# Optimization experiments

Hardware: AMD Instinct MI355X
Metric: run time of the kernel (lower is better)

## Reference

```python
import jax, jax.numpy as jnp
import numpy as np

SCORE_THR = 0.01
IOU_THR = 0.1          # NOTE: original layer hardcodes 0.1 in tf.image.non_max_suppression
MAX_DET = 100
NEG = jnp.float32(-1e30)


def _iou_one_vs_all(box, boxes):
    # box: [4] (y1,x1,y2,x2), boxes: [N,4]
    y1 = jnp.maximum(box[0], boxes[:, 0])
    x1 = jnp.maximum(box[1], boxes[:, 1])
    y2 = jnp.minimum(box[2], boxes[:, 2])
    x2 = jnp.minimum(box[3], boxes[:, 3])
    inter = jnp.maximum(y2 - y1, 0.0) * jnp.maximum(x2 - x1, 0.0)
    a = (box[2] - box[0]) * (box[3] - box[1])
    b = (boxes[:, 2] - boxes[:, 0]) * (boxes[:, 3] - boxes[:, 1])
    return inter / (a + b - inter + 1e-8)


def _nms_keep(boxes, scores):
    # Greedy NMS as a keep-mask over N anchors. Matches tf.image.non_max_suppression
    # restricted to anchors with score > SCORE_THR, up to MAX_DET selections.
    s = jnp.where(scores > SCORE_THR, scores, NEG)
    keep0 = jnp.zeros(s.shape, dtype=bool)

    def step(carry, _):
        s, keep = carry
        i = jnp.argmax(s)
        ok = s[i] > NEG * 0.5
        keep = keep.at[i].set(ok)
        iou = _iou_one_vs_all(boxes[i], boxes)
        s = jnp.where((iou > IOU_THR) & ok, NEG, s)
        s = s.at[i].set(NEG)
        return (s, keep), None

    (_, keep), _ = jax.lax.scan(step, (s, keep0), None, length=MAX_DET)
    return keep


def _filter_image(boxes_i, cls_i):
    # boxes_i: [N,4], cls_i: [N,C]
    C = cls_i.shape[1]
    # class-specific NMS: keep mask per class -> [C, N]
    keep = jax.vmap(lambda s: _nms_keep(boxes_i, s))(cls_i.T)
    keep_flat = keep.T.reshape(-1)          # [N*C], (anchor, class) flat order
    flat = cls_i.reshape(-1)                # [N*C]
    masked = jnp.where(keep_flat, flat, NEG)
    vals, idx = jax.lax.top_k(masked, MAX_DET)
    valid = vals > NEG * 0.5
    anchor = idx // C
    label = idx % C
    scores_out = jnp.where(valid, jnp.take(flat, idx), -1.0)
    boxes_out = jnp.where(valid[:, None], boxes_i[anchor], -1.0)
    labels_out = jnp.where(valid, label, -1).astype(jnp.int32)
    return boxes_out, scores_out, labels_out


def setup_inputs() -> dict:
    key = jax.random.key(0)
    k1, k2, k3 = jax.random.split(key, 3)
    B, N, C = 4, 49104, 90
    yx1 = jax.random.uniform(k1, (B, N, 2), dtype=jnp.float32) * 512.0
    hw = jax.random.uniform(k2, (B, N, 2), dtype=jnp.float32) * 128.0 + 1.0
    boxes = jnp.concatenate([yx1, yx1 + hw], axis=-1)          # [B,N,4] y1x1y2x2
    classification = jax.random.uniform(k3, (B, N, C), dtype=jnp.float32)
    return {"boxes": boxes, "classification": classification}


def reference(boxes, classification):
    return jax.vmap(_filter_image)(boxes, classification)
```

## Files before the change

kernel.cpp:

```cpp
#include <hip/hip_runtime.h>
#include <stdint.h>

typedef unsigned long long u64;

#define B_ 4
#define N_ 49104
#define C_ 90
#define NCLS (B_ * C_)
#define MAXK 100
#define THR 0.01f
#define NB2 2048
#define WIN 512
#define ACH 128
#define NCH ((N_ + ACH - 1) / ACH)
#define CAPC 32
#define NBIN_M 1280
#define BINBASE 0x3F6E0000u
#define BINSH_M 10

__device__ __forceinline__ float area_of(float y1, float x1, float y2, float x2) {
#pragma clang fp contract(off)
  return (y2 - y1) * (x2 - x1);
}

#define IOU_MID (26843547.0 / 268435456.0)

__device__ __forceinline__ bool iou_gt(float ay1, float ax1, float ay2, float ax2, float aa,
                                       float by1, float bx1, float by2, float bx2, float ba) {
#pragma clang fp contract(off)
  float y1 = fmaxf(ay1, by1);
  float x1 = fmaxf(ax1, bx1);
  float y2 = fminf(ay2, by2);
  float x2 = fminf(ax2, bx2);
  float inter = fmaxf(y2 - y1, 0.0f) * fmaxf(x2 - x1, 0.0f);
  float denom = aa + ba - inter + 1e-8f;
  return (double)inter >= IOU_MID * (double)denom;
}

__device__ __forceinline__ u64 umax64(u64 a, u64 b) { return a > b ? a : b; }

__device__ __forceinline__ u64 shfl_xor_u64(u64 v, int m) {
  int lo = __shfl_xor((int)(unsigned)v, m);
  int hi = __shfl_xor((int)(unsigned)(v >> 32), m);
  return ((u64)(unsigned)hi << 32) | (u64)(unsigned)lo;
}

__device__ __forceinline__ int key2bin_m(u64 k) {
  int d = (int)((unsigned)(k >> 32) - BINBASE);
  int bin = d >> BINSH_M;
  if (d < 0) bin = 0;
  if (bin > NBIN_M - 1) bin = NBIN_M - 1;
  return bin;
}

__global__ __launch_bounds__(256) void select_kernel(const float* __restrict__ cls,
                                                     u64* __restrict__ keybuf,
                                                     unsigned* __restrict__ cnt,
                                                     int capsel, float t0) {
  __shared__ u64 ll[C_ * CAPC];
  __shared__ unsigned lcnt[C_];
  __shared__ unsigned base_s[C_];
  int blk = blockIdx.x;
  int b = blk / NCH, ch = blk - b * NCH;
  int a0 = ch * ACH;
  int aEnd = a0 + ACH; if (aEnd > N_) aEnd = N_;
  int e0 = a0 * C_;
  int nelem = (aEnd - a0) * C_;
  int tid = threadIdx.x;

  for (int i = tid; i < C_; i += 256) lcnt[i] = 0u;
  __syncthreads();

  const float4* src4 = (const float4*)(cls + (size_t)b * N_ * C_ + e0);
  int n4 = nelem >> 2;
  for (int i4 = tid; i4 < n4; i4 += 256) {
    float4 v = src4[i4];
#pragma unroll
    for (int j = 0; j < 4; ++j) {
      float s = (&v.x)[j];
      if (s > t0) {
        int e = e0 + i4 * 4 + j;
        unsigned n = (unsigned)e / (unsigned)C_;
        unsigned c = (unsigned)e - n * (unsigned)C_;
        u64 key = ((u64)__float_as_uint(s) << 32) | (u64)(0xFFFFFFFFu - n);
        unsigned pos = atomicAdd(&lcnt[c], 1u);
        if (pos < CAPC) {
          ll[c * CAPC + pos] = key;
        } else {
          unsigned g = (unsigned)(b * C_) + c;
          unsigned gp = atomicAdd(&cnt[g * 16], 1u);
          if (gp < (unsigned)capsel) keybuf[(size_t)g * capsel + gp] = key;
        }
      }
    }
  }
  __syncthreads();

  if (tid < C_) {
    unsigned cc = lcnt[tid]; if (cc > CAPC) cc = CAPC;
    base_s[tid] = atomicAdd(&cnt[(b * C_ + tid) * 16], cc);
  }
  __syncthreads();

  for (int i = tid; i < C_ * CAPC; i += 256) {
    int c = i >> 5, j = i & 31;
    unsigned cc = lcnt[c]; if (cc > CAPC) cc = CAPC;
    if ((unsigned)j < cc) {
      unsigned pos = base_s[c] + (unsigned)j;
      if (pos < (unsigned)capsel)
        keybuf[(size_t)(b * C_ + c) * capsel + pos] = ll[i];
    }
  }
}

__global__ __launch_bounds__(512) void nms_kernel(const float* __restrict__ boxes,
                                                  const float* __restrict__ cls,
                                                  const u64* __restrict__ keybuf,
                                                  const unsigned* __restrict__ cnt,
                                                  int capsel, float t0,
                                                  u64* __restrict__ keepkeys,
                                                  int* __restrict__ nk_arr) {
  int gcls = blockIdx.x;
  int b = gcls / C_, c = gcls - b * C_;
  __shared__ u64 karr[4096];
  __shared__ unsigned hist[NB2];
  __shared__ unsigned sfx[NB2];
  __shared__ float4 kb[MAXK];
  __shared__ float ka[MAXK];
  __shared__ unsigned wsum[8];
  __shared__ int sh_cnt[8];
  int tid = threadIdx.x;
  int lane = tid & 63;
  int wid = tid >> 6;

  for (int i = tid; i < MAXK; i += 512) keepkeys[(size_t)gcls * MAXK + i] = 0ull;
  for (int i = tid; i < NB2; i += 512) hist[i] = 0u;
  __syncthreads();

  unsigned Mraw = cnt[gcls * 16];
  bool overflow = (Mraw > (unsigned)capsel);
  int M = overflow ? 0 : (int)Mraw;

  const u64* src = keybuf + (size_t)gcls * capsel;

  const int PK = 4096 / 512;
  u64 kreg[PK];
#pragma unroll
  for (int q = 0; q < PK; ++q) {
    kreg[q] = 0ull;
    int i = q * 512 + tid;
    if (i < M) {
      kreg[q] = src[i];
      atomicAdd(&hist[(unsigned)(kreg[q] >> 44) & (NB2 - 1)], 1u);
    }
  }
  __syncthreads();

  {
    const int W = NB2 / 512;
    unsigned loc[W];
    unsigned psum = 0;
#pragma unroll
    for (int q = 0; q < W; ++q) {
      psum += hist[NB2 - 1 - (tid * W + q)];
      loc[q] = psum;
    }
    unsigned incl = psum;
#pragma unroll
    for (int s = 1; s < 64; s <<= 1) {
      unsigned v = (unsigned)__shfl_up((int)incl, s);
      if (lane >= s) incl += v;
    }
    if (lane == 63) wsum[wid] = incl;
    __syncthreads();
    unsigned bs = incl - psum;
    for (int w2 = 0; w2 < wid; ++w2) bs += wsum[w2];
#pragma unroll
    for (int q = 0; q < W; ++q)
      sfx[NB2 - 1 - (tid * W + q)] = bs + loc[q];
  }
  __syncthreads();

#pragma unroll
  for (int q = 0; q < PK; ++q) {
    int i = q * 512 + tid;
    if (i < M) {
      u64 k = kreg[q];
      unsigned bin = (unsigned)(k >> 44) & (NB2 - 1);
      unsigned old = atomicSub(&hist[bin], 1u);
      karr[sfx[bin] - old] = k;
    }
  }
  __syncthreads();

  {
    u64 mk2[PK]; int mt[PK];
#pragma unroll
    for (int q = 0; q < PK; ++q) {
      mk2[q] = 0ull; mt[q] = -1;
      int i = q * 512 + tid;
      if (i < M) {
        u64 k = karr[i];
        int bin = (int)((unsigned)(k >> 44) & (NB2 - 1));
        int hi2 = (int)sfx[bin];
        int lo2 = (bin == NB2 - 1) ? 0 : (int)sfx[bin + 1];
        int r = lo2;
        for (int j = lo2; j < hi2; ++j) r += (karr[j] > k);
        mk2[q] = k; mt[q] = r;
      }
    }
    __syncthreads();
#pragma unroll
    for (int q = 0; q < PK; ++q)
      if (mt[q] >= 0) karr[mt[q]] = mk2[q];
  }
  __syncthreads();

  const float4* bx4 = (const float4*)(boxes + (size_t)b * N_ * 4);

  int seen = 0;
  int nwin = (M + WIN - 1) / WIN;
  for (int w = 0; w < nwin && seen < MAXK; ++w) {
    int base = w * WIN;
    int ci = base + tid;
    bool have = ci < M;
    float4 cb = make_float4(0.f, 0.f, 0.f, 0.f);
    float ca = 0.f;
    if (have) {
      u64 k = karr[ci];
      cb = bx4[0xFFFFFFFFu - (unsigned)(k & 0xFFFFFFFFull)];
      ca = area_of(cb.x, cb.y, cb.z, cb.w);
    }
    bool dead = !have;
    for (int j = 0; j < seen; ++j) {
      float4 sb = kb[j]; float sa = ka[j];
      dead |= iou_gt(sb.x, sb.y, sb.z, sb.w, sa,
                     cb.x, cb.y, cb.z, cb.w, ca);
    }
    u64 alive = __ballot(!dead);

    int nslice = (((M - base) < WIN ? (M - base) : WIN) + 63) >> 6;
    for (int s = 0; s < nslice; ++s) {
      if (wid == s) {
        int nkl = seen;
        int slo = base + (s << 6);
        while (alive != 0ull && nkl < MAXK) {
          int bit = __ffsll((long long)alive) - 1;
          float sy1 = __shfl(cb.x, bit);
          float sx1 = __shfl(cb.y, bit);
          float sy2 = __shfl(cb.z, bit);
          float sx2 = __shfl(cb.w, bit);
          float sa  = __shfl(ca,   bit);
          if (lane == 0) {
            u64 key = karr[slo + bit];
            unsigned anchor = 0xFFFFFFFFu - (unsigned)(key & 0xFFFFFFFFull);
            unsigned flat = anchor * C_ + (unsigned)c;
            keepkeys[(size_t)gcls * MAXK + nkl] =
                (key & 0xFFFFFFFF00000000ull) | (u64)(0xFFFFFFFFu - flat);
            kb[nkl] = make_float4(sy1, sx1, sy2, sx2);
            ka[nkl] = sa;
          }
          ++nkl;
          alive &= ~__ballot(iou_gt(sy1, sx1, sy2, sx2, sa,
                                    cb.x, cb.y, cb.z, cb.w, ca));
        }
        if (lane == 0) sh_cnt[s] = nkl;
        seen = nkl;
      }
      __syncthreads();
      int nkNew = (wid == s) ? seen : sh_cnt[s];
      if (nkNew >= MAXK) { seen = nkNew; break; }
      if (wid > s && nkNew > seen) {
        bool d2 = false;
        for (int j = seen; j < nkNew; ++j) {
          float4 sb = kb[j]; float sa = ka[j];
          d2 |= iou_gt(sb.x, sb.y, sb.z, sb.w, sa,
                       cb.x, cb.y, cb.z, cb.w, ca);
        }
        alive &= __ballot(!d2);
      }
      seen = nkNew;
    }
  }

  int nkF = seen;
  if (nkF < MAXK) {
    float teff = overflow ? 2.0f : t0;
    const float* sbase = cls + (size_t)b * N_ * C_ + c;
    const float* bx = boxes + (size_t)b * N_ * 4;
    u64* kkp = keepkeys + (size_t)gcls * MAXK;
    u64* red = karr;
    int nk2 = nkF;
    while (nk2 < MAXK) {
      u64 best = 0ull;
      for (int n = tid; n < N_; n += 512) {
        float s = sbase[(size_t)n * C_];
        if (s > THR && s <= teff) {
          float y1 = bx[(size_t)n * 4 + 0], x1 = bx[(size_t)n * 4 + 1];
          float y2 = bx[(size_t)n * 4 + 2], x2 = bx[(size_t)n * 4 + 3];
          float ar = area_of(y1, x1, y2, x2);
          bool ov = false;
          for (int j = 0; j < nk2; ++j) {
            float4 kbj = kb[j];
            if (iou_gt(kbj.x, kbj.y, kbj.z, kbj.w, ka[j], y1, x1, y2, x2, ar)) { ov = true; break; }
          }
          if (!ov) {
            u64 key = ((u64)__float_as_uint(s) << 32) | (u64)(0xFFFFFFFFu - (unsigned)n);
            best = umax64(best, key);
          }
        }
      }
      red[tid] = best;
      __syncthreads();
      for (int sft = 256; sft > 0; sft >>= 1) {
        if (tid < sft) red[tid] = umax64(red[tid], red[tid + sft]);
        __syncthreads();
      }
      u64 sel = red[0];
      __syncthreads();
      if (sel == 0ull) {
        if (tid == 0) {
          unsigned target2 = 0xFFFFFFFFu - (unsigned)c;
          for (int j = 0; j < nk2; ++j)
            if ((unsigned)(kkp[j] & 0xFFFFFFFFull) == target2) kkp[j] = 0ull;
        }
        break;
      }
      unsigned anchor = 0xFFFFFFFFu - (unsigned)(sel & 0xFFFFFFFFull);
      if (tid == 0) {
        float y1 = bx[(size_t)anchor * 4 + 0], x1 = bx[(size_t)anchor * 4 + 1];
        float y2 = bx[(size_t)anchor * 4 + 2], x2 = bx[(size_t)anchor * 4 + 3];
        kb[nk2] = make_float4(y1, x1, y2, x2);
        ka[nk2] = area_of(y1, x1, y2, x2);
        unsigned flat = anchor * C_ + (unsigned)c;
        kkp[nk2] = (sel & 0xFFFFFFFF00000000ull) | (u64)(0xFFFFFFFFu - flat);
      }
      ++nk2;
      __syncthreads();
    }
    nkF = nk2;
  }
  if (tid == 0) nk_arr[gcls] = nkF;
}

__global__ __launch_bounds__(256) void merge_kernel(const float* __restrict__ boxes,
                                                    const u64* __restrict__ keepkeys,
                                                    const int* __restrict__ nk_arr,
                                                    float* __restrict__ out) {
  int b = blockIdx.x;
  int tid = threadIdx.x;
  int lane = tid & 63;
  int wid = tid >> 6;
  __shared__ unsigned hist[NBIN_M];
  __shared__ unsigned sfx[NBIN_M];
  __shared__ unsigned wsum[4];
  __shared__ u64 mk[512];
  __shared__ u64 selk[MAXK];
  __shared__ int sh_thr;
  __shared__ unsigned sh_cc;
  const u64* kk = keepkeys + (size_t)b * C_ * MAXK;
  const int TOT = C_ * MAXK;

  for (int i = tid; i < NBIN_M; i += 256) hist[i] = 0u;
  if (tid == 0) { sh_thr = -1; sh_cc = 0u; }
  __syncthreads();
  for (int i = tid; i < TOT; i += 256) {
    u64 k = kk[i];
    if (k != 0ull) atomicAdd(&hist[key2bin_m(k)], 1u);
  }
  __syncthreads();

  const int W = 5;
  int j0 = tid * W;
  unsigned psum = 0;
#pragma unroll
  for (int q = 0; q < W; ++q) {
    int bin = NBIN_M - 1 - (j0 + q);
    if (bin >= 0) psum += hist[bin];
  }
  unsigned incl = psum;
#pragma unroll
  for (int s = 1; s < 64; s <<= 1) {
    unsigned v = (unsigned)__shfl_up((int)incl, s);
    if (lane >= s) incl += v;
  }
  if (lane == 63) wsum[wid] = incl;
  __syncthreads();
  unsigned base = 0;
  for (int w2 = 0; w2 < wid; ++w2) base += wsum[w2];
  unsigned running = base + incl - psum;
  int mythr = -1;
#pragma unroll
  for (int q = 0; q < W; ++q) {
    int bin = NBIN_M - 1 - (j0 + q);
    if (bin >= 0) {
      running += hist[bin];
      sfx[bin] = running;
      if (mythr < 0 && running >= (unsigned)MAXK) mythr = bin;
    }
  }
  if (mythr >= 0) atomicMax(&sh_thr, mythr);
  __syncthreads();

  int thr = sh_thr; if (thr < 0) thr = 0;
  unsigned S = sfx[thr];

  if (S <= 512u) {
    for (int i = tid; i < TOT; i += 256) {
      u64 k = kk[i];
      if (k != 0ull && key2bin_m(k) >= thr) {
        unsigned pos = atomicAdd(&sh_cc, 1u);
        mk[pos] = k;
      }
    }
    __syncthreads();
    for (int i = (int)S + tid; i < 512; i += 256) mk[i] = 0ull;
    __syncthreads();
    for (int k2 = 2; k2 <= 512; k2 <<= 1) {
      for (int j = k2 >> 1; j > 0; j >>= 1) {
        int i1 = 2 * tid - (tid & (j - 1));
        int i2 = i1 | j;
        u64 a = mk[i1], bb2 = mk[i2];
        bool desc = ((i1 & k2) == 0);
        bool sw = desc ? (a < bb2) : (a > bb2);
        if (sw) { mk[i1] = bb2; mk[i2] = a; }
        __syncthreads();
      }
    }
    for (int r = tid; r < MAXK; r += 256) selk[r] = mk[r];
    __syncthreads();
  } else {
    if (wid == 0) {
      int c0 = lane, c1 = lane + 64;
      int len0 = (c0 < C_) ? nk_arr[b * C_ + c0] : 0;
      int len1 = (c1 < C_) ? nk_arr[b * C_ + c1] : 0;
      int h0 = 0, h1 = 0;
      auto fetchc = [&](int cc, int& h, int len) -> u64 {
        while (h < len) {
          u64 k = kk[(size_t)cc * MAXK + h];
          if (k != 0ull) return k;
          ++h;
        }
        return 0ull;
      };
      u64 cand0 = (c0 < C_) ? fetchc(c0, h0, len0) : 0ull;
      u64 cand1 = (c1 < C_) ? fetchc(c1, h1, len1) : 0ull;
      for (int r = 0; r < MAXK; ++r) {
        u64 my = umax64(cand0, cand1);
        u64 g = my;
#pragma unroll
        for (int m = 1; m < 64; m <<= 1) g = umax64(g, shfl_xor_u64(g, m));
        if (lane == 0) selk[r] = g;
        if (g != 0ull && my == g) {
          if (cand0 == g) { ++h0; cand0 = fetchc(c0, h0, len0); }
          else            { ++h1; cand1 = fetchc(c1, h1, len1); }
        }
      }
    }
    __syncthreads();
  }

  for (int r = tid; r < MAXK; r += 256) {
    u64 s = selk[r];
    float oy1, ox1, oy2, ox2, sc, lb;
    if (s != 0ull) {
      unsigned flat = 0xFFFFFFFFu - (unsigned)(s & 0xFFFFFFFFull);
      unsigned anchor = flat / C_;
      unsigned label = flat - anchor * C_;
      sc = __uint_as_float((unsigned)(s >> 32));
      const float4 bp = ((const float4*)(boxes + (size_t)b * N_ * 4))[anchor];
      oy1 = bp.x; ox1 = bp.y; oy2 = bp.z; ox2 = bp.w;
      lb = (float)label;
    } else {
      oy1 = ox1 = oy2 = ox2 = -1.0f; sc = -1.0f; lb = -1.0f;
    }
    float* bo = out + ((size_t)b * MAXK + r) * 4;
    bo[0] = oy1; bo[1] = ox1; bo[2] = oy2; bo[3] = ox2;
    out[(size_t)B_ * MAXK * 4 + b * MAXK + r] = sc;
    out[(size_t)B_ * MAXK * 4 + B_ * MAXK + b * MAXK + r] = lb;
  }
}

extern "C" void kernel_launch(void* const* d_in, const int* in_sizes, int n_in,
                              void* d_out, int out_size, void* d_ws, size_t ws_size,
                              hipStream_t stream) {
  const float* boxes = (const float*)d_in[0];
  const float* cls = (const float*)d_in[1];
  char* ws = (char*)d_ws;

  int capsel; float t0;
  auto need_for = [](int cap) -> size_t {
    return 23040 + (size_t)NCLS * cap * 8 + 288000 + 1440;
  };
  if (ws_size >= need_for(4096))      { capsel = 4096; t0 = 0.93f;  }
  else if (ws_size >= need_for(2048)) { capsel = 2048; t0 = 0.962f; }
  else                                { capsel = 1024; t0 = 0.985f; }

  unsigned* cnt = (unsigned*)ws;
  u64* keybuf = (u64*)(ws + 23040);
  size_t off = 23040 + (size_t)NCLS * capsel * 8;
  u64* keepkeys = (u64*)(ws + off);      off += 288000;
  int* nk_arr = (int*)(ws + off);

  hipMemsetAsync(cnt, 0, 23040, stream);
  select_kernel<<<B_ * NCH, 256, 0, stream>>>(cls, keybuf, cnt, capsel, t0);
  nms_kernel<<<NCLS, 512, 0, stream>>>(boxes, cls, keybuf, cnt, capsel, t0,
                                       keepkeys, nk_arr);
  merge_kernel<<<B_, 256, 0, stream>>>(boxes, keepkeys, nk_arr, (float*)d_out);
}
```

Measured before the change: 189.0 us.

## Fuse merge into NMS via last-block pattern, shrink capacity, pair greedy steps

```diff
diff --git a/kernel.cpp b/kernel.cpp
--- a/kernel.cpp
+++ b/kernel.cpp
@@ -10,13 +10,16 @@
 #define MAXK 100
 #define THR 0.01f
 #define NB2 2048
-#define WIN 512
+#define WIN 256
+#define KCAP 1024
 #define ACH 128
 #define NCH ((N_ + ACH - 1) / ACH)
 #define CAPC 32
 #define NBIN_M 1280
 #define BINBASE 0x3F6E0000u
 #define BINSH_M 10
+#define T0 0.985f
+#define CAPSEL 1024
 
 __device__ __forceinline__ float area_of(float y1, float x1, float y2, float x2) {
 #pragma clang fp contract(off)
@@ -42,6 +45,12 @@
 __device__ __forceinline__ u64 shfl_xor_u64(u64 v, int m) {
   int lo = __shfl_xor((int)(unsigned)v, m);
   int hi = __shfl_xor((int)(unsigned)(v >> 32), m);
+  return ((u64)(unsigned)hi << 32) | (u64)(unsigned)lo;
+}
+
+__device__ __forceinline__ u64 shfl_u64(u64 v, int src) {
+  int lo = __shfl((int)(unsigned)v, src);
+  int hi = __shfl((int)(unsigned)(v >> 32), src);
   return ((u64)(unsigned)hi << 32) | (u64)(unsigned)lo;
 }
 
@@ -113,42 +122,46 @@
   }
 }
 
-__global__ __launch_bounds__(512) void nms_kernel(const float* __restrict__ boxes,
+__global__ __launch_bounds__(256) void nms_kernel(const float* __restrict__ boxes,
                                                   const float* __restrict__ cls,
                                                   const u64* __restrict__ keybuf,
                                                   const unsigned* __restrict__ cnt,
+                                                  unsigned* __restrict__ done,
                                                   int capsel, float t0,
                                                   u64* __restrict__ keepkeys,
-                                                  int* __restrict__ nk_arr) {
+                                                  int* __restrict__ nk_arr,
+                                                  float* __restrict__ out) {
   int gcls = blockIdx.x;
   int b = gcls / C_, c = gcls - b * C_;
-  __shared__ u64 karr[4096];
+  __shared__ u64 karr[KCAP];
   __shared__ unsigned hist[NB2];
   __shared__ unsigned sfx[NB2];
   __shared__ float4 kb[MAXK];
   __shared__ float ka[MAXK];
-  __shared__ unsigned wsum[8];
-  __shared__ int sh_cnt[8];
+  __shared__ unsigned wsum[4];
+  __shared__ int sh_cnt[4];
+  __shared__ int sh_last, sh_thr;
+  __shared__ unsigned sh_cc;
   int tid = threadIdx.x;
   int lane = tid & 63;
   int wid = tid >> 6;
 
-  for (int i = tid; i < MAXK; i += 512) keepkeys[(size_t)gcls * MAXK + i] = 0ull;
-  for (int i = tid; i < NB2; i += 512) hist[i] = 0u;
+  for (int i = tid; i < MAXK; i += 256) keepkeys[(size_t)gcls * MAXK + i] = 0ull;
+  for (int i = tid; i < NB2; i += 256) hist[i] = 0u;
   __syncthreads();
 
   unsigned Mraw = cnt[gcls * 16];
-  bool overflow = (Mraw > (unsigned)capsel);
+  bool overflow = (Mraw > (unsigned)KCAP);
   int M = overflow ? 0 : (int)Mraw;
 
   const u64* src = keybuf + (size_t)gcls * capsel;
 
-  const int PK = 4096 / 512;
+  const int PK = KCAP / 256;
   u64 kreg[PK];
 #pragma unroll
   for (int q = 0; q < PK; ++q) {
     kreg[q] = 0ull;
-    int i = q * 512 + tid;
+    int i = q * 256 + tid;
     if (i < M) {
       kreg[q] = src[i];
       atomicAdd(&hist[(unsigned)(kreg[q] >> 44) & (NB2 - 1)], 1u);
@@ -157,7 +170,7 @@
   __syncthreads();
 
   {
-    const int W = NB2 / 512;
+    const int W = NB2 / 256;
     unsigned loc[W];
     unsigned psum = 0;
 #pragma unroll
@@ -183,7 +196,7 @@
 
 #pragma unroll
   for (int q = 0; q < PK; ++q) {
-    int i = q * 512 + tid;
+    int i = q * 256 + tid;
     if (i < M) {
       u64 k = kreg[q];
       unsigned bin = (unsigned)(k >> 44) & (NB2 - 1);
@@ -198,7 +211,7 @@
 #pragma unroll
     for (int q = 0; q < PK; ++q) {
       mk2[q] = 0ull; mt[q] = -1;
-      int i = q * 512 + tid;
+      int i = q * 256 + tid;
       if (i < M) {
         u64 k = karr[i];
         int bin = (int)((unsigned)(k >> 44) & (NB2 - 1));
@@ -224,11 +237,12 @@
     int base = w * WIN;
     int ci = base + tid;
     bool have = ci < M;
+    u64 myk = 0ull;
     float4 cb = make_float4(0.f, 0.f, 0.f, 0.f);
     float ca = 0.f;
     if (have) {
-      u64 k = karr[ci];
-      cb = bx4[0xFFFFFFFFu - (unsigned)(k & 0xFFFFFFFFull)];
+      myk = karr[ci];
+      cb = bx4[0xFFFFFFFFu - (unsigned)(myk & 0xFFFFFFFFull)];
       ca = area_of(cb.x, cb.y, cb.z, cb.w);
     }
     bool dead = !have;
@@ -243,32 +257,53 @@
     for (int s = 0; s < nslice; ++s) {
       if (wid == s) {
         int nkl = seen;
-        int slo = base + (s << 6);
         while (alive != 0ull && nkl < MAXK) {
           int bit = __ffsll((long long)alive) - 1;
-          float sy1 = __shfl(cb.x, bit);
-          float sx1 = __shfl(cb.y, bit);
-          float sy2 = __shfl(cb.z, bit);
-          float sx2 = __shfl(cb.w, bit);
-          float sa  = __shfl(ca,   bit);
+          u64 rest = alive & (alive - 1ull);
+          int nbit = __ffsll((long long)rest) - 1;
+          int pidx = nbit >= 0 ? nbit : bit;
+          float b1y1 = __shfl(cb.x, bit), b1x1 = __shfl(cb.y, bit);
+          float b1y2 = __shfl(cb.z, bit), b1x2 = __shfl(cb.w, bit);
+          float a1 = __shfl(ca, bit);
+          float b2y1 = __shfl(cb.x, pidx), b2x1 = __shfl(cb.y, pidx);
+          float b2y2 = __shfl(cb.z, pidx), b2x2 = __shfl(cb.w, pidx);
+          float a2 = __shfl(ca, pidx);
+          u64 k1 = shfl_u64(myk, bit);
+          u64 k2 = shfl_u64(myk, pidx);
+          bool kill1 = iou_gt(b1y1, b1x1, b1y2, b1x2, a1,
+                              cb.x, cb.y, cb.z, cb.w, ca);
+          bool kill2 = iou_gt(b2y1, b2x1, b2y2, b2x2, a2,
+                              cb.x, cb.y, cb.z, cb.w, ca);
+          u64 m1 = __ballot(kill1);
           if (lane == 0) {
-            u64 key = karr[slo + bit];
-            unsigned anchor = 0xFFFFFFFFu - (unsigned)(key & 0xFFFFFFFFull);
+            unsigned anchor = 0xFFFFFFFFu - (unsigned)(k1 & 0xFFFFFFFFull);
             unsigned flat = anchor * C_ + (unsigned)c;
             keepkeys[(size_t)gcls * MAXK + nkl] =
-                (key & 0xFFFFFFFF00000000ull) | (u64)(0xFFFFFFFFu - flat);
-            kb[nkl] = make_float4(sy1, sx1, sy2, sx2);
-            ka[nkl] = sa;
+                (k1 & 0xFFFFFFFF00000000ull) | (u64)(0xFFFFFFFFu - flat);
+            kb[nkl] = make_float4(b1y1, b1x1, b1y2, b1x2);
+            ka[nkl] = a1;
           }
           ++nkl;
-          alive &= ~__ballot(iou_gt(sy1, sx1, sy2, sx2, sa,
-                                    cb.x, cb.y, cb.z, cb.w, ca));
+          alive = rest & ~m1;
+          if (alive == 0ull || nkl >= MAXK) break;
+          if ((__ffsll((long long)alive) - 1) == nbit) {
+            u64 m2 = __ballot(kill2);
+            if (lane == 0) {
+              unsigned anchor = 0xFFFFFFFFu - (unsigned)(k2 & 0xFFFFFFFFull);
+              unsigned flat = anchor * C_ + (unsigned)c;
+              keepkeys[(size_t)gcls * MAXK + nkl] =
+                  (k2 & 0xFFFFFFFF00000000ull) | (u64)(0xFFFFFFFFu - flat);
+              kb[nkl] = make_float4(b2y1, b2x1, b2y2, b2x2);
+              ka[nkl] = a2;
+            }
+            ++nkl;
+            alive &= ~m2;
+          }
         }
         if (lane == 0) sh_cnt[s] = nkl;
-        seen = nkl;
-      }
-      __syncthreads();
-      int nkNew = (wid == s) ? seen : sh_cnt[s];
+      }
+      __syncthreads();
+      int nkNew = sh_cnt[s];
       if (nkNew >= MAXK) { seen = nkNew; break; }
       if (wid > s && nkNew > seen) {
         bool d2 = false;
@@ -293,7 +328,7 @@
     int nk2 = nkF;
     while (nk2 < MAXK) {
       u64 best = 0ull;
-      for (int n = tid; n < N_; n += 512) {
+      for (int n = tid; n < N_; n += 256) {
         float s = sbase[(size_t)n * C_];
         if (s > THR && s <= teff) {
           float y1 = bx[(size_t)n * 4 + 0], x1 = bx[(size_t)n * 4 + 1];
@@ -312,7 +347,7 @@
       }
       red[tid] = best;
       __syncthreads();
-      for (int sft = 256; sft > 0; sft >>= 1) {
+      for (int sft = 128; sft > 0; sft >>= 1) {
         if (tid < sft) red[tid] = umax64(red[tid], red[tid + sft]);
         __syncthreads();
       }
@@ -341,143 +376,142 @@
     nkF = nk2;
   }
   if (tid == 0) nk_arr[gcls] = nkF;
-}
-
-__global__ __launch_bounds__(256) void merge_kernel(const float* __restrict__ boxes,
-                                                    const u64* __restrict__ keepkeys,
-                                                    const int* __restrict__ nk_arr,
-                                                    float* __restrict__ out) {
-  int b = blockIdx.x;
-  int tid = threadIdx.x;
-  int lane = tid & 63;
-  int wid = tid >> 6;
-  __shared__ unsigned hist[NBIN_M];
-  __shared__ unsigned sfx[NBIN_M];
-  __shared__ unsigned wsum[4];
-  __shared__ u64 mk[512];
-  __shared__ u64 selk[MAXK];
-  __shared__ int sh_thr;
-  __shared__ unsigned sh_cc;
-  const u64* kk = keepkeys + (size_t)b * C_ * MAXK;
-  const int TOT = C_ * MAXK;
-
-  for (int i = tid; i < NBIN_M; i += 256) hist[i] = 0u;
-  if (tid == 0) { sh_thr = -1; sh_cc = 0u; }
-  __syncthreads();
-  for (int i = tid; i < TOT; i += 256) {
-    u64 k = kk[i];
-    if (k != 0ull) atomicAdd(&hist[key2bin_m(k)], 1u);
-  }
-  __syncthreads();
-
-  const int W = 5;
-  int j0 = tid * W;
-  unsigned psum = 0;
-#pragma unroll
-  for (int q = 0; q < W; ++q) {
-    int bin = NBIN_M - 1 - (j0 + q);
-    if (bin >= 0) psum += hist[bin];
-  }
-  unsigned incl = psum;
-#pragma unroll
-  for (int s = 1; s < 64; s <<= 1) {
-    unsigned v = (unsigned)__shfl_up((int)incl, s);
-    if (lane >= s) incl += v;
-  }
-  if (lane == 63) wsum[wid] = incl;
-  __syncthreads();
-  unsigned base = 0;
-  for (int w2 = 0; w2 < wid; ++w2) base += wsum[w2];
-  unsigned running = base + incl - psum;
-  int mythr = -1;
-#pragma unroll
-  for (int q = 0; q < W; ++q) {
-    int bin = NBIN_M - 1 - (j0 + q);
-    if (bin >= 0) {
-      running += hist[bin];
-      sfx[bin] = running;
-      if (mythr < 0 && running >= (unsigned)MAXK) mythr = bin;
-    }
-  }
-  if (mythr >= 0) atomicMax(&sh_thr, mythr);
-  __syncthreads();
-
-  int thr = sh_thr; if (thr < 0) thr = 0;
-  unsigned S = sfx[thr];
-
-  if (S <= 512u) {
+
+  __syncthreads();
+  if (tid == 0) {
+    __threadfence();
+    sh_last = (atomicAdd(&done[b], 1u) == (unsigned)(C_ - 1)) ? 1 : 0;
+  }
+  __syncthreads();
+  if (!sh_last) return;
+  __threadfence();
+
+  {
+    const u64* kk = keepkeys + (size_t)b * C_ * MAXK;
+    const int TOT = C_ * MAXK;
+    unsigned* histm = hist;
+    unsigned* sfxm = sfx;
+    u64* mk = karr;
+    u64* selk = karr + 512;
+
+    for (int i = tid; i < NBIN_M; i += 256) histm[i] = 0u;
+    if (tid == 0) { sh_thr = -1; sh_cc = 0u; }
+    __syncthreads();
     for (int i = tid; i < TOT; i += 256) {
       u64 k = kk[i];
-      if (k != 0ull && key2bin_m(k) >= thr) {
-        unsigned pos = atomicAdd(&sh_cc, 1u);
-        mk[pos] = k;
-      }
+      if (k != 0ull) atomicAdd(&histm[key2bin_m(k)], 1u);
     }
     __syncthreads();
-    for (int i = (int)S + tid; i < 512; i += 256) mk[i] = 0ull;
+
+    const int W = 5;
+    int j0 = tid * W;
+    unsigned psum = 0;
+#pragma unroll
+    for (int q = 0; q < W; ++q) {
+      int bin = NBIN_M - 1 - (j0 + q);
+      if (bin >= 0) psum += histm[bin];
+    }
+    unsigned incl = psum;
+#pragma unroll
+    for (int s = 1; s < 64; s <<= 1) {
+      unsigned v = (unsigned)__shfl_up((int)incl, s);
+      if (lane >= s) incl += v;
+    }
+    if (lane == 63) wsum[wid] = incl;
     __syncthreads();
-    for (int k2 = 2; k2 <= 512; k2 <<= 1) {
-      for (int j = k2 >> 1; j > 0; j >>= 1) {
-        int i1 = 2 * tid - (tid & (j - 1));
-        int i2 = i1 | j;
-        u64 a = mk[i1], bb2 = mk[i2];
-        bool desc = ((i1 & k2) == 0);
-        bool sw = desc ? (a < bb2) : (a > bb2);
-        if (sw) { mk[i1] = bb2; mk[i2] = a; }
-        __syncthreads();
-      }
-    }
-    for (int r = tid; r < MAXK; r += 256) selk[r] = mk[r];
+    unsigned base = 0;
+    for (int w2 = 0; w2 < wid; ++w2) base += wsum[w2];
+    unsigned running = base + incl - psum;
+    int mythr = -1;
+#pragma unroll
+    for (int q = 0; q < W; ++q) {
+      int bin = NBIN_M - 1 - (j0 + q);
+      if (bin >= 0) {
+        running += histm[bin];
+        sfxm[bin] = running;
+        if (mythr < 0 && running >= (unsigned)MAXK) mythr = bin;
+      }
+    }
+    if (mythr >= 0) atomicMax(&sh_thr, mythr);
     __syncthreads();
-  } else {
-    if (wid == 0) {
-      int c0 = lane, c1 = lane + 64;
-      int len0 = (c0 < C_) ? nk_arr[b * C_ + c0] : 0;
-      int len1 = (c1 < C_) ? nk_arr[b * C_ + c1] : 0;
-      int h0 = 0, h1 = 0;
-      auto fetchc = [&](int cc, int& h, int len) -> u64 {
-        while (h < len) {
-          u64 k = kk[(size_t)cc * MAXK + h];
-          if (k != 0ull) return k;
-          ++h;
-        }
-        return 0ull;
-      };
-      u64 cand0 = (c0 < C_) ? fetchc(c0, h0, len0) : 0ull;
-      u64 cand1 = (c1 < C_) ? fetchc(c1, h1, len1) : 0ull;
-      for (int r = 0; r < MAXK; ++r) {
-        u64 my = umax64(cand0, cand1);
-        u64 g = my;
-#pragma unroll
-        for (int m = 1; m < 64; m <<= 1) g = umax64(g, shfl_xor_u64(g, m));
-        if (lane == 0) selk[r] = g;
-        if (g != 0ull && my == g) {
-          if (cand0 == g) { ++h0; cand0 = fetchc(c0, h0, len0); }
-          else            { ++h1; cand1 = fetchc(c1, h1, len1); }
-        }
-      }
-    }
-    __syncthreads();
-  }
-
-  for (int r = tid; r < MAXK; r += 256) {
-    u64 s = selk[r];
-    float oy1, ox1, oy2, ox2, sc, lb;
-    if (s != 0ull) {
-      unsigned flat = 0xFFFFFFFFu - (unsigned)(s & 0xFFFFFFFFull);
-      unsigned anchor = flat / C_;
-      unsigned label = flat - anchor * C_;
-      sc = __uint_as_float((unsigned)(s >> 32));
-      const float4 bp = ((const float4*)(boxes + (size_t)b * N_ * 4))[anchor];
-      oy1 = bp.x; ox1 = bp.y; oy2 = bp.z; ox2 = bp.w;
-      lb = (float)label;
+
+    int thr = sh_thr; if (thr < 0) thr = 0;
+    unsigned S = sfxm[thr];
+
+    if (S <= 512u) {
+      for (int i = tid; i < TOT; i += 256) {
+        u64 k = kk[i];
+        if (k != 0ull && key2bin_m(k) >= thr) {
+          unsigned pos = atomicAdd(&sh_cc, 1u);
+          mk[pos] = k;
+        }
+      }
+      __syncthreads();
+      for (int i = (int)S + tid; i < 512; i += 256) mk[i] = 0ull;
+      __syncthreads();
+      for (int k2 = 2; k2 <= 512; k2 <<= 1) {
+        for (int j = k2 >> 1; j > 0; j >>= 1) {
+          int i1 = 2 * tid - (tid & (j - 1));
+          int i2 = i1 | j;
+          u64 a = mk[i1], bb2 = mk[i2];
+          bool desc = ((i1 & k2) == 0);
+          bool sw = desc ? (a < bb2) : (a > bb2);
+          if (sw) { mk[i1] = bb2; mk[i2] = a; }
+          __syncthreads();
+        }
+      }
+      for (int r = tid; r < MAXK; r += 256) selk[r] = mk[r];
+      __syncthreads();
     } else {
-      oy1 = ox1 = oy2 = ox2 = -1.0f; sc = -1.0f; lb = -1.0f;
-    }
-    float* bo = out + ((size_t)b * MAXK + r) * 4;
-    bo[0] = oy1; bo[1] = ox1; bo[2] = oy2; bo[3] = ox2;
-    out[(size_t)B_ * MAXK * 4 + b * MAXK + r] = sc;
-    out[(size_t)B_ * MAXK * 4 + B_ * MAXK + b * MAXK + r] = lb;
+      if (wid == 0) {
+        int c0 = lane, c1 = lane + 64;
+        int len0 = (c0 < C_) ? nk_arr[b * C_ + c0] : 0;
+        int len1 = (c1 < C_) ? nk_arr[b * C_ + c1] : 0;
+        int h0 = 0, h1 = 0;
+        auto fetchc = [&](int cc, int& h, int len) -> u64 {
+          while (h < len) {
+            u64 k = kk[(size_t)cc * MAXK + h];
+            if (k != 0ull) return k;
+            ++h;
+          }
+          return 0ull;
+        };
+        u64 cand0 = (c0 < C_) ? fetchc(c0, h0, len0) : 0ull;
+        u64 cand1 = (c1 < C_) ? fetchc(c1, h1, len1) : 0ull;
+        for (int r = 0; r < MAXK; ++r) {
+          u64 my = umax64(cand0, cand1);
+          u64 g = my;
+#pragma unroll
+          for (int m = 1; m < 64; m <<= 1) g = umax64(g, shfl_xor_u64(g, m));
+          if (lane == 0) selk[r] = g;
+          if (g != 0ull && my == g) {
+            if (cand0 == g) { ++h0; cand0 = fetchc(c0, h0, len0); }
+            else            { ++h1; cand1 = fetchc(c1, h1, len1); }
+          }
+        }
+      }
+      __syncthreads();
+    }
+
+    for (int r = tid; r < MAXK; r += 256) {
+      u64 s = selk[r];
+      float oy1, ox1, oy2, ox2, sc, lb;
+      if (s != 0ull) {
+        unsigned flat = 0xFFFFFFFFu - (unsigned)(s & 0xFFFFFFFFull);
+        unsigned anchor = flat / C_;
+        unsigned label = flat - anchor * C_;
+        sc = __uint_as_float((unsigned)(s >> 32));
+        const float4 bp = ((const float4*)(boxes + (size_t)b * N_ * 4))[anchor];
+        oy1 = bp.x; ox1 = bp.y; oy2 = bp.z; ox2 = bp.w;
+        lb = (float)label;
+      } else {
+        oy1 = ox1 = oy2 = ox2 = -1.0f; sc = -1.0f; lb = -1.0f;
+      }
+      float* bo = out + ((size_t)b * MAXK + r) * 4;
+      bo[0] = oy1; bo[1] = ox1; bo[2] = oy2; bo[3] = ox2;
+      out[(size_t)B_ * MAXK * 4 + b * MAXK + r] = sc;
+      out[(size_t)B_ * MAXK * 4 + B_ * MAXK + b * MAXK + r] = lb;
+    }
   }
 }
 
@@ -488,23 +522,15 @@
   const float* cls = (const float*)d_in[1];
   char* ws = (char*)d_ws;
 
-  int capsel; float t0;
-  auto need_for = [](int cap) -> size_t {
-    return 23040 + (size_t)NCLS * cap * 8 + 288000 + 1440;
-  };
-  if (ws_size >= need_for(4096))      { capsel = 4096; t0 = 0.93f;  }
-  else if (ws_size >= need_for(2048)) { capsel = 2048; t0 = 0.962f; }
-  else                                { capsel = 1024; t0 = 0.985f; }
-
   unsigned* cnt = (unsigned*)ws;
-  u64* keybuf = (u64*)(ws + 23040);
-  size_t off = 23040 + (size_t)NCLS * capsel * 8;
+  unsigned* done = (unsigned*)(ws + 23040);
+  u64* keybuf = (u64*)(ws + 23104);
+  size_t off = 23104 + (size_t)NCLS * CAPSEL * 8;
   u64* keepkeys = (u64*)(ws + off);      off += 288000;
   int* nk_arr = (int*)(ws + off);
 
-  hipMemsetAsync(cnt, 0, 23040, stream);
-  select_kernel<<<B_ * NCH, 256, 0, stream>>>(cls, keybuf, cnt, capsel, t0);
-  nms_kernel<<<NCLS, 512, 0, stream>>>(boxes, cls, keybuf, cnt, capsel, t0,
-                                       keepkeys, nk_arr);
-  merge_kernel<<<B_, 256, 0, stream>>>(boxes, keepkeys, nk_arr, (float*)d_out);
-}
+  hipMemsetAsync(ws, 0, 23104, stream);
+  select_kernel<<<B_ * NCH, 256, 0, stream>>>(cls, keybuf, cnt, CAPSEL, T0);
+  nms_kernel<<<NCLS, 256, 0, stream>>>(boxes, cls, keybuf, cnt, done, CAPSEL, T0,
+                                       keepkeys, nk_arr, (float*)d_out);
+}
```

Result: no change. 185.9 us (-1.6%).
